# Kernel optimization log

Measured on AMD Instinct MI355X. Metric: run time of the kernel, lower is better.

Reference implementation:

```python
import jax, jax.numpy as jnp
import numpy as np

L, N, E, H = 1024, 8, 512, 8


def setup_inputs() -> dict:
    key = jax.random.key(0)
    k1, k2, k3, k4 = jax.random.split(key, 4)
    query = jax.random.normal(k1, (L, N, E), dtype=jnp.float32)
    time = jax.random.normal(k2, (L, N, 1), dtype=jnp.float32) * 1000.0  # timestamps
    in_proj_weight = jax.random.normal(k3, (3 * E, E), dtype=jnp.float32) * 0.02
    in_proj_bias = jnp.zeros((3 * E,), dtype=jnp.float32)
    out_proj_weight = jax.random.normal(k4, (E, E), dtype=jnp.float32) * 0.02
    out_proj_bias = jnp.zeros((E,), dtype=jnp.float32)
    return {
        "query": query,
        "time": time,
        "in_proj_weight": in_proj_weight,
        "in_proj_bias": in_proj_bias,
        "out_proj_weight": out_proj_weight,
        "out_proj_bias": out_proj_bias,
    }


def _temporal_mha(query, time, in_proj_weight, in_proj_bias, out_proj_weight, out_proj_bias):
    # Self-attention path of temporal_multi_head_attention_forward (query is key is value).
    tgt_len, bsz, embed_dim = query.shape
    num_heads = H
    head_dim = embed_dim // num_heads
    scaling = float(head_dim) ** -0.5

    # Temporal bias: tt = time.permute(1,0,2) -> (N, L, 1); alpha[b,i,j] = exp((t_bi - t_bj)/1e6)
    tt = jnp.transpose(time, (1, 0, 2))  # (N, L, 1)
    alpha_time = jnp.exp((tt - jnp.reshape(tt, (bsz, 1, tgt_len))) / 1.0e6)  # (N, L, L)

    # Fused in-projection then chunk into q, k, v.
    qkv = query @ in_proj_weight.T + in_proj_bias  # (L, N, 3E)
    q, k, v = jnp.split(qkv, 3, axis=-1)
    q = q * scaling

    def heads(x):  # (L, N, E) -> (N, H, L, hd)
        return jnp.transpose(x.reshape(tgt_len, bsz, num_heads, head_dim), (1, 2, 0, 3))

    q, k, v = heads(q), heads(k), heads(v)

    # Scores with temporal bias injected (broadcast over heads) -- this is the
    # materialized (N, H, L, L) tensor that breaks the SDPA fusion path.
    scores = jnp.einsum("bhld,bhsd->bhls", q, k) * alpha_time[:, None, :, :]
    attn = jax.nn.softmax(scores, axis=-1)  # dropout_p = 0.0 (inference/reference)

    out = jnp.einsum("bhls,bhsd->bhld", attn, v)  # (N, H, L, hd)
    out = jnp.transpose(out, (2, 0, 1, 3)).reshape(tgt_len, bsz, embed_dim)  # (L, N, E)
    return out @ out_proj_weight.T + out_proj_bias


def reference(query, time, in_proj_weight, in_proj_bias, out_proj_weight, out_proj_bias):
    return _temporal_mha(query, time, in_proj_weight, in_proj_bias, out_proj_weight, out_proj_bias)
```

## Files before the change

kernel.cpp:

```cpp
#include <hip/hip_runtime.h>
#include <cstdint>
#include <cstddef>

typedef unsigned short u16;
typedef unsigned int u32;
typedef __attribute__((ext_vector_type(8))) short short8;
typedef __attribute__((ext_vector_type(4))) float f32x4;
typedef __attribute__((ext_vector_type(16))) float f32x16;

#define L_SEQ 1024
#define N_B   8
#define E_DIM 512
#define H_H   8
#define D_H   64
#define M_ROWS 8192

__device__ __forceinline__ u16 f2bf(float f) {
    u32 u = __float_as_uint(f);
    u32 r = (u + 0x7fffu + ((u >> 16) & 1u)) >> 16;
    return (u16)r;
}

__device__ __forceinline__ void gload16(const void* g, void* l) {
    __builtin_amdgcn_global_load_lds(
        (__attribute__((address_space(1))) void*)(g),
        (__attribute__((address_space(3))) void*)(l), 16, 0, 0);
}

__device__ __forceinline__ short8 ldsw(const u16* base, int row, int c) {
    return *reinterpret_cast<const short8*>(
        reinterpret_cast<const char*>(base) + row * 128 + ((c ^ (row & 7)) << 4));
}

__global__ __launch_bounds__(256) void convert_kernel(
    const float* __restrict__ a, const float* __restrict__ b, const float* __restrict__ c,
    u16* __restrict__ ab, u16* __restrict__ bb, u16* __restrict__ cb)
{
    const int NA = M_ROWS * E_DIM / 4;
    const int NB = 1536 * E_DIM / 4;
    const int i4 = blockIdx.x * 256 + threadIdx.x;
    const float* src; u16* dst; int j;
    if (i4 < NA)           { src = a; dst = ab; j = i4; }
    else if (i4 < NA + NB) { src = b; dst = bb; j = i4 - NA; }
    else                   { src = c; dst = cb; j = i4 - NA - NB; }
    const float4 v = reinterpret_cast<const float4*>(src)[j];
    ushort4 o;
    o.x = f2bf(v.x); o.y = f2bf(v.y); o.z = f2bf(v.z); o.w = f2bf(v.w);
    reinterpret_cast<ushort4*>(dst)[j] = o;
}

template <int MODE>
__global__ __launch_bounds__(256, 2) void gemm_kernel(
    const u16* __restrict__ A, const u16* __restrict__ B,
    const float* __restrict__ bias, const float* __restrict__ tptr,
    u16* __restrict__ qh, u16* __restrict__ kh, u16* __restrict__ vh,
    float* __restrict__ outf)
{
    __shared__ __align__(16) u16 Asm[128 * 64];
    __shared__ __align__(16) u16 Bsm[128 * 64];
    const int tid = threadIdx.x;
    const int lane = tid & 63, w = tid >> 6;
    const int wm = w >> 1, wn = w & 1;
    const int m0 = blockIdx.x * 128, n0 = blockIdx.y * 128;

    f32x4 acc[4][4];
    #pragma unroll
    for (int mi = 0; mi < 4; ++mi)
        #pragma unroll
        for (int ni = 0; ni < 4; ++ni)
            #pragma unroll
            for (int r = 0; r < 4; ++r) acc[mi][ni][r] = 0.f;

    const int srow = (w << 3) + (lane >> 3);
    const int csrc = ((lane & 7) ^ (lane >> 3)) << 3;

    for (int kt = 0; kt < 8; ++kt) {
        __syncthreads();
        #pragma unroll
        for (int i = 0; i < 4; ++i) {
            const int row = (i << 5) + srow;
            gload16(A + (size_t)(m0 + row) * 512 + (kt << 6) + csrc,
                    (char*)Asm + (i << 12) + (w << 10));
            gload16(B + (size_t)(n0 + row) * 512 + (kt << 6) + csrc,
                    (char*)Bsm + (i << 12) + (w << 10));
        }
        __syncthreads();
        #pragma unroll
        for (int k01 = 0; k01 < 2; ++k01) {
            short8 af[4], bfr[4];
            #pragma unroll
            for (int x = 0; x < 4; ++x) {
                af[x]  = ldsw(Asm, (wm << 6) + (x << 4) + (lane & 15), (k01 << 2) + (lane >> 4));
                bfr[x] = ldsw(Bsm, (wn << 6) + (x << 4) + (lane & 15), (k01 << 2) + (lane >> 4));
            }
            #pragma unroll
            for (int mi = 0; mi < 4; ++mi)
                #pragma unroll
                for (int ni = 0; ni < 4; ++ni)
                    acc[mi][ni] = __builtin_amdgcn_mfma_f32_16x16x32_bf16(
                        af[mi], bfr[ni], acc[mi][ni], 0, 0, 0);
        }
    }

    const int nb = n0 + (wn << 6) + (lane & 15);
    const int mb = m0 + (wm << 6) + ((lane >> 4) << 2);
    float bsv[4];
    #pragma unroll
    for (int ni = 0; ni < 4; ++ni) bsv[ni] = bias[nb + (ni << 4)];
    const int sec = n0 >> 9;

    #pragma unroll
    for (int mi = 0; mi < 4; ++mi) {
        #pragma unroll
        for (int r = 0; r < 4; ++r) {
            const int m = mb + (mi << 4) + r;
            float scale = 1.f;
            if (MODE == 0) {
                if (sec == 0)      scale = 0.125f * __expf(tptr[m] * 1e-6f);
                else if (sec == 1) scale = __expf(tptr[m] * -1e-6f);
            }
            #pragma unroll
            for (int ni = 0; ni < 4; ++ni) {
                const int n = nb + (ni << 4);
                const float v = acc[mi][ni][r] + bsv[ni];
                if (MODE == 0) {
                    const int l_seq = m >> 3, bb2 = m & 7;
                    const int hh = (n & 511) >> 6, dd = n & 63;
                    u16* dst = (sec == 0) ? qh : (sec == 1) ? kh : vh;
                    dst[(((size_t)(bb2 << 3) + hh) * L_SEQ + l_seq) * D_H + dd] = f2bf(v * scale);
                } else {
                    outf[(size_t)m * 512 + n] = v;
                }
            }
        }
    }
}

__global__ __launch_bounds__(256) void transpose_v(
    const u16* __restrict__ vh, u16* __restrict__ vt)
{
    __shared__ __align__(16) u16 T[64 * 64];
    const int bh = blockIdx.x, kt = blockIdx.y;
    const u16* src = vh + ((size_t)bh * L_SEQ + kt * 64) * D_H;

    #pragma unroll
    for (int rnd = 0; rnd < 2; ++rnd) {
        const int slot = rnd * 256 + threadIdx.x;
        const int row = slot >> 3, c = slot & 7;
        const uint4 v = *reinterpret_cast<const uint4*>(src + row * 64 + c * 8);
        const int cs = c ^ (row & 7) ^ ((row >> 3) & 7);
        *reinterpret_cast<uint4*>(&T[row * 64 + cs * 8]) = v;
    }
    __syncthreads();
    #pragma unroll
    for (int rnd = 0; rnd < 2; ++rnd) {
        const int slot = rnd * 256 + threadIdx.x;
        const int d = slot >> 3, kc = slot & 7;
        u16 tmp[8];
        #pragma unroll
        for (int j = 0; j < 8; ++j) {
            const int row = kc * 8 + j;
            const int col = (((d >> 3) ^ (row & 7) ^ ((row >> 3) & 7)) << 3) + (d & 7);
            tmp[j] = T[row * 64 + col];
        }
        *reinterpret_cast<uint4*>(vt + ((size_t)bh * D_H + d) * L_SEQ + kt * 64 + kc * 8) =
            *reinterpret_cast<uint4*>(tmp);
    }
}

__global__ __launch_bounds__(256, 2) void attn_kernel(
    const u16* __restrict__ qh, const u16* __restrict__ kh,
    const u16* __restrict__ vt, u16* __restrict__ ao)
{
    __shared__ __align__(16) float SMEMf[8448];
    u16* Ksm = reinterpret_cast<u16*>(SMEMf);
    u16* Vsm = Ksm + 4096;

    const int tid = threadIdx.x;
    const int lane = tid & 63, w = tid >> 6;
    const int hi = lane >> 5, q31 = lane & 31;
    const int bh = blockIdx.x, qt = blockIdx.y;
    const int b = bh >> 3, h = bh & 7;

    const u16* qrow = qh + ((size_t)bh * L_SEQ + qt * 128 + w * 32 + q31) * D_H;
    short8 qf[4];
    #pragma unroll
    for (int ks = 0; ks < 4; ++ks)
        qf[ks] = *reinterpret_cast<const short8*>(qrow + ks * 16 + hi * 8);

    f32x16 oacc[2];
    #pragma unroll
    for (int d = 0; d < 2; ++d)
        #pragma unroll
        for (int r = 0; r < 16; ++r) oacc[d][r] = 0.f;
    float m_run = -1e30f, l_run = 0.f;

    const u16* kbase = kh + (size_t)bh * L_SEQ * D_H;
    const u16* vbase = vt + (size_t)bh * D_H * L_SEQ;
    const int srow = (w << 3) + (lane >> 3);
    const int csrc = ((lane & 7) ^ (lane >> 3)) << 3;

    for (int kt = 0; kt < 16; ++kt) {
        __syncthreads();
        #pragma unroll
        for (int i = 0; i < 2; ++i) {
            const int row = i * 32 + srow;
            gload16(kbase + (size_t)(kt * 64 + row) * 64 + csrc,
                    (char*)Ksm + (i << 12) + (w << 10));
            gload16(vbase + (size_t)row * L_SEQ + kt * 64 + csrc,
                    (char*)Vsm + (i << 12) + (w << 10));
        }
        __syncthreads();

        f32x16 s[2];
        #pragma unroll
        for (int d = 0; d < 2; ++d)
            #pragma unroll
            for (int r = 0; r < 16; ++r) s[d][r] = 0.f;
        #pragma unroll
        for (int ks = 0; ks < 4; ++ks) {
            const int c = 2 * ks + hi;
            const short8 ka0 = ldsw(Ksm, q31, c);
            const short8 ka1 = ldsw(Ksm, 32 + q31, c);
            s[0] = __builtin_amdgcn_mfma_f32_32x32x16_bf16(ka0, qf[ks], s[0], 0, 0, 0);
            s[1] = __builtin_amdgcn_mfma_f32_32x32x16_bf16(ka1, qf[ks], s[1], 0, 0, 0);
        }

        float mx = -1e30f;
        #pragma unroll
        for (int hh = 0; hh < 2; ++hh)
            #pragma unroll
            for (int r = 0; r < 16; ++r) mx = fmaxf(mx, s[hh][r]);
        mx = fmaxf(mx, __shfl_xor(mx, 32));
        const float mn = fmaxf(m_run, mx);
        const float fr = __expf(m_run - mn);
        float p[2][16];
        float sum = 0.f;
        #pragma unroll
        for (int hh = 0; hh < 2; ++hh)
            #pragma unroll
            for (int r = 0; r < 16; ++r) {
                const float e = __expf(s[hh][r] - mn);
                p[hh][r] = e; sum += e;
            }
        sum += __shfl_xor(sum, 32);
        l_run = l_run * fr + sum;
        m_run = mn;
        #pragma unroll
        for (int d = 0; d < 2; ++d) oacc[d] *= fr;

        #pragma unroll
        for (int ks = 0; ks < 4; ++ks) {
            const int e = ks & 1, hh = ks >> 1;
            const u32 pkA = (u32)f2bf(p[hh][8 * e + 0]) | ((u32)f2bf(p[hh][8 * e + 1]) << 16);
            const u32 pkB = (u32)f2bf(p[hh][8 * e + 2]) | ((u32)f2bf(p[hh][8 * e + 3]) << 16);
            const u32 pkC = (u32)f2bf(p[hh][8 * e + 4]) | ((u32)f2bf(p[hh][8 * e + 5]) << 16);
            const u32 pkD = (u32)f2bf(p[hh][8 * e + 6]) | ((u32)f2bf(p[hh][8 * e + 7]) << 16);
            const u32 keep0 = hi ? pkC : pkA, keep1 = hi ? pkD : pkB;
            const u32 send0 = hi ? pkA : pkC, send1 = hi ? pkB : pkD;
            const u32 r0 = (u32)__shfl_xor((int)send0, 32);
            const u32 r1 = (u32)__shfl_xor((int)send1, 32);
            union { u32 u[4]; short8 v; } pf;
            pf.u[0] = hi ? r0 : keep0;  pf.u[1] = hi ? r1 : keep1;
            pf.u[2] = hi ? keep0 : r0;  pf.u[3] = hi ? keep1 : r1;
            const int c = 2 * ks + hi;
            const short8 va0 = ldsw(Vsm, q31, c);
            const short8 va1 = ldsw(Vsm, 32 + q31, c);
            oacc[0] = __builtin_amdgcn_mfma_f32_32x32x16_bf16(va0, pf.v, oacc[0], 0, 0, 0);
            oacc[1] = __builtin_amdgcn_mfma_f32_32x32x16_bf16(va1, pf.v, oacc[1], 0, 0, 0);
        }
    }

    __syncthreads();
    const float inv = 1.f / l_run;
    float* myO = SMEMf + w * 2080;
    #pragma unroll
    for (int dh = 0; dh < 2; ++dh)
        #pragma unroll
        for (int r = 0; r < 16; ++r) {
            const int d = dh * 32 + (r & 3) + 8 * (r >> 2) + 4 * hi;
            myO[q31 * 65 + d] = oacc[dh][r] * inv;
        }
    __syncthreads();
    #pragma unroll
    for (int i = 0; i < 4; ++i) {
        const int slot = i * 64 + lane;
        const int qq = slot >> 3, dc = slot & 7;
        u16 outv[8];
        #pragma unroll
        for (int j = 0; j < 8; ++j) outv[j] = f2bf(myO[qq * 65 + dc * 8 + j]);
        const int lrow = qt * 128 + w * 32 + qq;
        *reinterpret_cast<uint4*>(ao + ((size_t)lrow * N_B + b) * E_DIM + h * 64 + dc * 8) =
            *reinterpret_cast<uint4*>(outv);
    }
}

extern "C" void kernel_launch(void* const* d_in, const int* in_sizes, int n_in,
                              void* d_out, int out_size, void* d_ws, size_t ws_size,
                              hipStream_t stream) {
    const float* query = (const float*)d_in[0];
    const float* timep = (const float*)d_in[1];
    const float* w_in  = (const float*)d_in[2];
    const float* b_in  = (const float*)d_in[3];
    const float* w_out = (const float*)d_in[4];
    const float* b_out = (const float*)d_in[5];
    float* out = (float*)d_out;

    u16* ws = (u16*)d_ws;
    const size_t SZ = (size_t)M_ROWS * E_DIM;
    u16* Abf  = ws;
    u16* Wibf = Abf + SZ;
    u16* Wobf = Wibf + 1536 * 512;
    u16* qhb  = Wobf + 512 * 512;
    u16* khb  = qhb + SZ;
    u16* vhb  = khb + SZ;
    u16* vtb  = vhb + SZ;
    u16* aob  = vtb + SZ;

    convert_kernel<<<5120, 256, 0, stream>>>(query, w_in, w_out, Abf, Wibf, Wobf);
    gemm_kernel<0><<<dim3(64, 12), 256, 0, stream>>>(
        Abf, Wibf, b_in, timep, qhb, khb, vhb, nullptr);
    transpose_v<<<dim3(64, 16), 256, 0, stream>>>(vhb, vtb);
    attn_kernel<<<dim3(64, 8), 256, 0, stream>>>(qhb, khb, vtb, aob);
    gemm_kernel<1><<<dim3(64, 4), 256, 0, stream>>>(
        aob, Wobf, b_out, nullptr, nullptr, nullptr, nullptr, out);
}
```

Measured before the change: 143.5 us.

## Double-buffer attention K/V loads, use exp2 softmax with lazy rescale, retile GEMMs

The attention kernel switches to 128-thread blocks over 64-query tiles and double-buffers K/V tiles in LDS, so the next tile's global loads overlap the current tile's compute with one barrier per iteration. Softmax now uses exp2, with log2(e) folded into the query scale. The running-max rescale is skipped unless the max grows by more than 8, and P is packed with the hardware bf16 pack instruction. The GEMM gains a templated M tile, with the output projection using a 64-row tile to double its block count, and MFMA sections are wrapped in setprio. The lazy rescale trades some numerical headroom for fewer exps and multiplies, and the smaller attention blocks change occupancy and the number of K/V reloads per query.

```diff
diff --git a/kernel.cpp b/kernel.cpp
--- a/kernel.cpp
+++ b/kernel.cpp
@@ -15,10 +15,22 @@
 #define D_H   64
 #define M_ROWS 8192
 
+#if __has_builtin(__builtin_amdgcn_exp2f)
+#define EXP2(x) __builtin_amdgcn_exp2f(x)
+#else
+#define EXP2(x) exp2f(x)
+#endif
+
 __device__ __forceinline__ u16 f2bf(float f) {
     u32 u = __float_as_uint(f);
     u32 r = (u + 0x7fffu + ((u >> 16) & 1u)) >> 16;
     return (u16)r;
+}
+
+__device__ __forceinline__ u32 cvtpk(float lo, float hi_) {
+    u32 r;
+    asm("v_cvt_pk_bf16_f32 %0, %1, %2" : "=v"(r) : "v"(lo), "v"(hi_));
+    return r;
 }
 
 __device__ __forceinline__ void gload16(const void* g, void* l) {
@@ -49,23 +61,24 @@
     reinterpret_cast<ushort4*>(dst)[j] = o;
 }
 
-template <int MODE>
+template <int MODE, int MI>
 __global__ __launch_bounds__(256, 2) void gemm_kernel(
     const u16* __restrict__ A, const u16* __restrict__ B,
     const float* __restrict__ bias, const float* __restrict__ tptr,
     u16* __restrict__ qh, u16* __restrict__ kh, u16* __restrict__ vh,
     float* __restrict__ outf)
 {
-    __shared__ __align__(16) u16 Asm[128 * 64];
+    constexpr int BM = MI * 32;
+    __shared__ __align__(16) u16 Asm_[BM * 64];
     __shared__ __align__(16) u16 Bsm[128 * 64];
     const int tid = threadIdx.x;
     const int lane = tid & 63, w = tid >> 6;
     const int wm = w >> 1, wn = w & 1;
-    const int m0 = blockIdx.x * 128, n0 = blockIdx.y * 128;
-
-    f32x4 acc[4][4];
-    #pragma unroll
-    for (int mi = 0; mi < 4; ++mi)
+    const int m0 = blockIdx.x * BM, n0 = blockIdx.y * 128;
+
+    f32x4 acc[MI][4];
+    #pragma unroll
+    for (int mi = 0; mi < MI; ++mi)
         #pragma unroll
         for (int ni = 0; ni < 4; ++ni)
             #pragma unroll
@@ -77,46 +90,55 @@
     for (int kt = 0; kt < 8; ++kt) {
         __syncthreads();
         #pragma unroll
+        for (int i = 0; i < MI; ++i) {
+            const int row = (i << 5) + srow;
+            gload16(A + (size_t)(m0 + row) * 512 + (kt << 6) + csrc,
+                    (char*)Asm_ + (i << 12) + (w << 10));
+        }
+        #pragma unroll
         for (int i = 0; i < 4; ++i) {
             const int row = (i << 5) + srow;
-            gload16(A + (size_t)(m0 + row) * 512 + (kt << 6) + csrc,
-                    (char*)Asm + (i << 12) + (w << 10));
             gload16(B + (size_t)(n0 + row) * 512 + (kt << 6) + csrc,
                     (char*)Bsm + (i << 12) + (w << 10));
         }
         __syncthreads();
         #pragma unroll
         for (int k01 = 0; k01 < 2; ++k01) {
-            short8 af[4], bfr[4];
-            #pragma unroll
-            for (int x = 0; x < 4; ++x) {
-                af[x]  = ldsw(Asm, (wm << 6) + (x << 4) + (lane & 15), (k01 << 2) + (lane >> 4));
-                bfr[x] = ldsw(Bsm, (wn << 6) + (x << 4) + (lane & 15), (k01 << 2) + (lane >> 4));
-            }
-            #pragma unroll
-            for (int mi = 0; mi < 4; ++mi)
+            short8 af[MI], bfr[4];
+            #pragma unroll
+            for (int x = 0; x < MI; ++x)
+                af[x] = ldsw(Asm_, wm * (MI * 16) + (x << 4) + (lane & 15),
+                             (k01 << 2) + (lane >> 4));
+            #pragma unroll
+            for (int x = 0; x < 4; ++x)
+                bfr[x] = ldsw(Bsm, (wn << 6) + (x << 4) + (lane & 15),
+                              (k01 << 2) + (lane >> 4));
+            __builtin_amdgcn_s_setprio(1);
+            #pragma unroll
+            for (int mi = 0; mi < MI; ++mi)
                 #pragma unroll
                 for (int ni = 0; ni < 4; ++ni)
                     acc[mi][ni] = __builtin_amdgcn_mfma_f32_16x16x32_bf16(
                         af[mi], bfr[ni], acc[mi][ni], 0, 0, 0);
+            __builtin_amdgcn_s_setprio(0);
         }
     }
 
     const int nb = n0 + (wn << 6) + (lane & 15);
-    const int mb = m0 + (wm << 6) + ((lane >> 4) << 2);
+    const int mb = m0 + wm * (MI * 16) + ((lane >> 4) << 2);
     float bsv[4];
     #pragma unroll
     for (int ni = 0; ni < 4; ++ni) bsv[ni] = bias[nb + (ni << 4)];
     const int sec = n0 >> 9;
 
     #pragma unroll
-    for (int mi = 0; mi < 4; ++mi) {
+    for (int mi = 0; mi < MI; ++mi) {
         #pragma unroll
         for (int r = 0; r < 4; ++r) {
             const int m = mb + (mi << 4) + r;
             float scale = 1.f;
             if (MODE == 0) {
-                if (sec == 0)      scale = 0.125f * __expf(tptr[m] * 1e-6f);
+                if (sec == 0)      scale = 0.18033688f * __expf(tptr[m] * 1e-6f);
                 else if (sec == 1) scale = __expf(tptr[m] * -1e-6f);
             }
             #pragma unroll
@@ -168,13 +190,11 @@
     }
 }
 
-__global__ __launch_bounds__(256, 2) void attn_kernel(
+__global__ __launch_bounds__(128) void attn_kernel(
     const u16* __restrict__ qh, const u16* __restrict__ kh,
     const u16* __restrict__ vt, u16* __restrict__ ao)
 {
-    __shared__ __align__(16) float SMEMf[8448];
-    u16* Ksm = reinterpret_cast<u16*>(SMEMf);
-    u16* Vsm = Ksm + 4096;
+    __shared__ __align__(16) u16 SM[16384];
 
     const int tid = threadIdx.x;
     const int lane = tid & 63, w = tid >> 6;
@@ -182,7 +202,7 @@
     const int bh = blockIdx.x, qt = blockIdx.y;
     const int b = bh >> 3, h = bh & 7;
 
-    const u16* qrow = qh + ((size_t)bh * L_SEQ + qt * 128 + w * 32 + q31) * D_H;
+    const u16* qrow = qh + ((size_t)bh * L_SEQ + qt * 64 + w * 32 + q31) * D_H;
     short8 qf[4];
     #pragma unroll
     for (int ks = 0; ks < 4; ++ks)
@@ -197,65 +217,78 @@
 
     const u16* kbase = kh + (size_t)bh * L_SEQ * D_H;
     const u16* vbase = vt + (size_t)bh * D_H * L_SEQ;
-    const int srow = (w << 3) + (lane >> 3);
-    const int csrc = ((lane & 7) ^ (lane >> 3)) << 3;
+    const int r8 = lane >> 3;
+    const int csrc = ((lane & 7) ^ r8) << 3;
+
+    auto stage = [&](int buf, int kt) {
+        #pragma unroll
+        for (int i = 0; i < 4; ++i) {
+            const int row = (w << 5) + (i << 3) + r8;
+            gload16(kbase + (size_t)(kt * 64 + row) * 64 + csrc,
+                    (char*)SM + buf * 8192 + (w << 12) + (i << 10));
+            gload16(vbase + (size_t)row * 1024 + kt * 64 + csrc,
+                    (char*)SM + 16384 + buf * 8192 + (w << 12) + (i << 10));
+        }
+    };
+
+    int cur = 0;
+    stage(0, 0);
+    __syncthreads();
 
     for (int kt = 0; kt < 16; ++kt) {
-        __syncthreads();
-        #pragma unroll
-        for (int i = 0; i < 2; ++i) {
-            const int row = i * 32 + srow;
-            gload16(kbase + (size_t)(kt * 64 + row) * 64 + csrc,
-                    (char*)Ksm + (i << 12) + (w << 10));
-            gload16(vbase + (size_t)row * L_SEQ + kt * 64 + csrc,
-                    (char*)Vsm + (i << 12) + (w << 10));
-        }
-        __syncthreads();
+        if (kt < 15) stage(cur ^ 1, kt + 1);
+        const u16* Kc = SM + cur * 4096;
+        const u16* Vc = SM + 8192 + cur * 4096;
 
         f32x16 s[2];
         #pragma unroll
         for (int d = 0; d < 2; ++d)
             #pragma unroll
             for (int r = 0; r < 16; ++r) s[d][r] = 0.f;
+        __builtin_amdgcn_s_setprio(1);
         #pragma unroll
         for (int ks = 0; ks < 4; ++ks) {
             const int c = 2 * ks + hi;
-            const short8 ka0 = ldsw(Ksm, q31, c);
-            const short8 ka1 = ldsw(Ksm, 32 + q31, c);
+            const short8 ka0 = ldsw(Kc, q31, c);
+            const short8 ka1 = ldsw(Kc, 32 + q31, c);
             s[0] = __builtin_amdgcn_mfma_f32_32x32x16_bf16(ka0, qf[ks], s[0], 0, 0, 0);
             s[1] = __builtin_amdgcn_mfma_f32_32x32x16_bf16(ka1, qf[ks], s[1], 0, 0, 0);
         }
-
-        float mx = -1e30f;
+        __builtin_amdgcn_s_setprio(0);
+
+        float pmax = -1e30f;
         #pragma unroll
         for (int hh = 0; hh < 2; ++hh)
             #pragma unroll
-            for (int r = 0; r < 16; ++r) mx = fmaxf(mx, s[hh][r]);
-        mx = fmaxf(mx, __shfl_xor(mx, 32));
-        const float mn = fmaxf(m_run, mx);
-        const float fr = __expf(m_run - mn);
+            for (int r = 0; r < 16; ++r) pmax = fmaxf(pmax, s[hh][r]);
+        pmax = fmaxf(pmax, __shfl_xor(pmax, 32));
+        if (!__all(pmax - m_run <= 8.0f)) {
+            const float mn = fmaxf(m_run, pmax);
+            const float fr = EXP2(m_run - mn);
+            l_run *= fr;
+            oacc[0] *= fr; oacc[1] *= fr;
+            m_run = mn;
+        }
         float p[2][16];
         float sum = 0.f;
         #pragma unroll
         for (int hh = 0; hh < 2; ++hh)
             #pragma unroll
             for (int r = 0; r < 16; ++r) {
-                const float e = __expf(s[hh][r] - mn);
+                const float e = EXP2(s[hh][r] - m_run);
                 p[hh][r] = e; sum += e;
             }
         sum += __shfl_xor(sum, 32);
-        l_run = l_run * fr + sum;
-        m_run = mn;
-        #pragma unroll
-        for (int d = 0; d < 2; ++d) oacc[d] *= fr;
-
+        l_run += sum;
+
+        __builtin_amdgcn_s_setprio(1);
         #pragma unroll
         for (int ks = 0; ks < 4; ++ks) {
             const int e = ks & 1, hh = ks >> 1;
-            const u32 pkA = (u32)f2bf(p[hh][8 * e + 0]) | ((u32)f2bf(p[hh][8 * e + 1]) << 16);
-            const u32 pkB = (u32)f2bf(p[hh][8 * e + 2]) | ((u32)f2bf(p[hh][8 * e + 3]) << 16);
-            const u32 pkC = (u32)f2bf(p[hh][8 * e + 4]) | ((u32)f2bf(p[hh][8 * e + 5]) << 16);
-            const u32 pkD = (u32)f2bf(p[hh][8 * e + 6]) | ((u32)f2bf(p[hh][8 * e + 7]) << 16);
+            const u32 pkA = cvtpk(p[hh][8 * e + 0], p[hh][8 * e + 1]);
+            const u32 pkB = cvtpk(p[hh][8 * e + 2], p[hh][8 * e + 3]);
+            const u32 pkC = cvtpk(p[hh][8 * e + 4], p[hh][8 * e + 5]);
+            const u32 pkD = cvtpk(p[hh][8 * e + 6], p[hh][8 * e + 7]);
             const u32 keep0 = hi ? pkC : pkA, keep1 = hi ? pkD : pkB;
             const u32 send0 = hi ? pkA : pkC, send1 = hi ? pkB : pkD;
             const u32 r0 = (u32)__shfl_xor((int)send0, 32);
@@ -264,16 +297,18 @@
             pf.u[0] = hi ? r0 : keep0;  pf.u[1] = hi ? r1 : keep1;
             pf.u[2] = hi ? keep0 : r0;  pf.u[3] = hi ? keep1 : r1;
             const int c = 2 * ks + hi;
-            const short8 va0 = ldsw(Vsm, q31, c);
-            const short8 va1 = ldsw(Vsm, 32 + q31, c);
+            const short8 va0 = ldsw(Vc, q31, c);
+            const short8 va1 = ldsw(Vc, 32 + q31, c);
             oacc[0] = __builtin_amdgcn_mfma_f32_32x32x16_bf16(va0, pf.v, oacc[0], 0, 0, 0);
             oacc[1] = __builtin_amdgcn_mfma_f32_32x32x16_bf16(va1, pf.v, oacc[1], 0, 0, 0);
         }
-    }
-
-    __syncthreads();
+        __builtin_amdgcn_s_setprio(0);
+        __syncthreads();
+        cur ^= 1;
+    }
+
     const float inv = 1.f / l_run;
-    float* myO = SMEMf + w * 2080;
+    float* myO = (float*)SM + w * 2080;
     #pragma unroll
     for (int dh = 0; dh < 2; ++dh)
         #pragma unroll
@@ -289,7 +324,7 @@
         u16 outv[8];
         #pragma unroll
         for (int j = 0; j < 8; ++j) outv[j] = f2bf(myO[qq * 65 + dc * 8 + j]);
-        const int lrow = qt * 128 + w * 32 + qq;
+        const int lrow = qt * 64 + w * 32 + qq;
         *reinterpret_cast<uint4*>(ao + ((size_t)lrow * N_B + b) * E_DIM + h * 64 + dc * 8) =
             *reinterpret_cast<uint4*>(outv);
     }
@@ -318,10 +353,10 @@
     u16* aob  = vtb + SZ;
 
     convert_kernel<<<5120, 256, 0, stream>>>(query, w_in, w_out, Abf, Wibf, Wobf);
-    gemm_kernel<0><<<dim3(64, 12), 256, 0, stream>>>(
+    gemm_kernel<0, 4><<<dim3(64, 12), 256, 0, stream>>>(
         Abf, Wibf, b_in, timep, qhb, khb, vhb, nullptr);
     transpose_v<<<dim3(64, 16), 256, 0, stream>>>(vhb, vtb);
-    attn_kernel<<<dim3(64, 8), 256, 0, stream>>>(qhb, khb, vtb, aob);
-    gemm_kernel<1><<<dim3(64, 4), 256, 0, stream>>>(
+    attn_kernel<<<dim3(64, 16), 128, 0, stream>>>(qhb, khb, vtb, aob);
+    gemm_kernel<1, 2><<<dim3(128, 4), 256, 0, stream>>>(
         aob, Wobf, b_out, nullptr, nullptr, nullptr, nullptr, out);
 }
```

New measurement: 142.7 us. Within noise of the previous version (-0.6%).
